# Kernel tuning notes

Measured on AMD Instinct MI355X. Metric: run time of the kernel, lower is better.

Reference implementation:

```python
import jax, jax.numpy as jnp
import numpy as np

N_NODES = 50000
N_EDGES = 1600000
F_IN = 128
HID = 128
N_CLS = 16


def setup_inputs() -> dict:
    key = jax.random.key(0)
    ks = jax.random.split(key, 8)
    x = jax.random.normal(ks[0], (N_NODES, F_IN), dtype=jnp.float32)
    edge_index = jax.random.randint(ks[1], (2, N_EDGES), 0, N_NODES, dtype=jnp.int64)
    W1 = jax.random.normal(ks[2], (F_IN, HID), dtype=jnp.float32) * (1.0 / np.sqrt(F_IN))
    b1 = jnp.zeros((HID,), dtype=jnp.float32)
    W2 = jax.random.normal(ks[3], (HID, HID), dtype=jnp.float32) * (1.0 / np.sqrt(HID))
    b2 = jnp.zeros((HID,), dtype=jnp.float32)
    W3 = jax.random.normal(ks[4], (HID, N_CLS), dtype=jnp.float32) * (1.0 / np.sqrt(HID))
    b3 = jnp.zeros((N_CLS,), dtype=jnp.float32)
    return {"x": x, "edge_index": edge_index, "W1": W1, "b1": b1,
            "W2": W2, "b2": b2, "W3": W3, "b3": b3}


def _gcn_norm(edge_index, n_nodes, dtype):
    # PyG gcn_norm with add_self_loops=True, improved=False
    loops = jnp.arange(n_nodes, dtype=edge_index.dtype)
    row = jnp.concatenate([edge_index[0], loops])  # source j
    col = jnp.concatenate([edge_index[1], loops])  # target i
    deg = jax.ops.segment_sum(jnp.ones(row.shape[0], dtype=dtype), col,
                              num_segments=n_nodes)
    dinv = jnp.where(deg > 0, jax.lax.rsqrt(deg), 0.0)
    norm = dinv[row] * dinv[col]  # [E + N]
    return row, col, norm


def _gcn_conv(h, W, b, row, col, norm, n_nodes):
    h = h @ W                              # [N, out] linear first (PyG order)
    msg = h[row] * norm[:, None]           # gather + per-edge scale
    agg = jax.ops.segment_sum(msg, col, num_segments=n_nodes)  # scatter-add
    return agg + b


def reference(x, edge_index, W1, b1, W2, b2, W3, b3):
    n = x.shape[0]
    row, col, norm = _gcn_norm(edge_index, n, x.dtype)
    h = jax.nn.relu(_gcn_conv(x, W1, b1, row, col, norm, n))
    h = jax.nn.relu(_gcn_conv(h, W2, b2, row, col, norm, n))
    h = jax.nn.relu(_gcn_conv(h, W3, b3, row, col, norm, n))
    return h
```

## Files before the change

kernel.cpp:

```cpp
#include <hip/hip_runtime.h>
#include <hip/hip_fp16.h>


static inline int cdiv(int a, int b) { return (a + b - 1) / b; }

__global__ __launch_bounds__(256) void k_zero_int(int* p, int n) {
    int i = blockIdx.x * 256 + threadIdx.x;
    if (i < n) p[i] = 0;
}

__global__ __launch_bounds__(256) void k_count(const int* __restrict__ col, int* cnt, int e) {
    int i = blockIdx.x * 256 + threadIdx.x;
    if (i < e) atomicAdd(&cnt[col[i]], 1);
}

__global__ __launch_bounds__(256) void k_scanA(const int* __restrict__ cnt, int* bsum,
                                               float* __restrict__ dinv, int n) {
    __shared__ int s[256];
    int t = threadIdx.x;
    int i = blockIdx.x * 256 + t;
    int v = (i < n) ? cnt[i] : 0;
    if (i < n) dinv[i] = rsqrtf((float)(v + 1));
    s[t] = v;
    __syncthreads();
    for (int off = 128; off > 0; off >>= 1) {
        if (t < off) s[t] += s[t + off];
        __syncthreads();
    }
    if (t == 0) bsum[blockIdx.x] = s[0];
}

__global__ __launch_bounds__(256) void k_scanB(int* bsum, int nb) {
    __shared__ int s[256];
    int t = threadIdx.x;
    int v = (t < nb) ? bsum[t] : 0;
    s[t] = v;
    for (int off = 1; off < 256; off <<= 1) {
        __syncthreads();
        int x = (t >= off) ? s[t - off] : 0;
        __syncthreads();
        s[t] += x;
    }
    __syncthreads();
    if (t < nb) bsum[t] = s[t] - v;
}

__global__ __launch_bounds__(256) void k_scanC(const int* __restrict__ cnt, const int* __restrict__ bsum,
                                               int* offs, int* cur, int n) {
    __shared__ int s[256];
    int t = threadIdx.x;
    int i = blockIdx.x * 256 + t;
    int v = (i < n) ? cnt[i] : 0;
    s[t] = v;
    for (int off = 1; off < 256; off <<= 1) {
        __syncthreads();
        int x = (t >= off) ? s[t - off] : 0;
        __syncthreads();
        s[t] += x;
    }
    __syncthreads();
    int ov = bsum[blockIdx.x] + s[t] - v;
    if (i <= n) offs[i] = ov;
    if (i < n) cur[i] = ov;
}

__global__ __launch_bounds__(256) void k_fill_xcd(const int* __restrict__ row, const int* __restrict__ col,
                                                  const float* __restrict__ dinv, int* cur,
                                                  unsigned int* __restrict__ csr, int e, int n, int nblk) {
    int g = blockIdx.x & 7;
    int b = blockIdx.x >> 3;
    int rs = (n + 7) >> 3;
    int lo = g * rs;
    int hi = min(lo + rs, n);
    int stride = nblk * 256;
    for (int i = b * 256 + threadIdx.x; i < e; i += stride) {
        int c = col[i];
        if (c >= lo && c < hi) {
            int r = row[i];
            float w = dinv[r] * dinv[c];
            int pos = atomicAdd(&cur[c], 1);
            unsigned short hw = __half_as_ushort(__float2half_rn(w));
            csr[pos] = ((unsigned int)r << 16) | (unsigned int)hw;
        }
    }
}

__global__ __launch_bounds__(256) void k_gemm128(const float* __restrict__ X, const float* __restrict__ W,
                                                 __half* __restrict__ Ah, int n) {
    __shared__ float sW[128 * 128];
    __shared__ float sX[16][128];
    int tid = threadIdx.x;
    for (int i = tid; i < 4096; i += 256)
        ((float4*)sW)[i] = ((const float4*)W)[i];

    int row0 = blockIdx.x * 128;
    int tx = tid & 15, ty = tid >> 4;
    float acc[8][8];
    #pragma unroll
    for (int i = 0; i < 8; ++i)
        #pragma unroll
        for (int j = 0; j < 8; ++j) acc[i][j] = 0.f;

    for (int k0 = 0; k0 < 128; k0 += 16) {
        __syncthreads();
        #pragma unroll
        for (int i = tid; i < 512; i += 256) {
            int r = i >> 2, kq = i & 3;
            int gr = row0 + r;
            float4 v = (gr < n) ? ((const float4*)X)[(size_t)gr * 32 + (k0 >> 2) + kq]
                                : make_float4(0.f, 0.f, 0.f, 0.f);
            sX[kq * 4 + 0][r] = v.x;
            sX[kq * 4 + 1][r] = v.y;
            sX[kq * 4 + 2][r] = v.z;
            sX[kq * 4 + 3][r] = v.w;
        }
        __syncthreads();
        #pragma unroll
        for (int kk = 0; kk < 16; ++kk) {
            float a[8], b[8];
            *(float4*)&a[0] = *(const float4*)&sX[kk][ty * 8];
            *(float4*)&a[4] = *(const float4*)&sX[kk][ty * 8 + 4];
            *(float4*)&b[0] = *(const float4*)&sW[(k0 + kk) * 128 + tx * 8];
            *(float4*)&b[4] = *(const float4*)&sW[(k0 + kk) * 128 + tx * 8 + 4];
            #pragma unroll
            for (int i = 0; i < 8; ++i)
                #pragma unroll
                for (int j = 0; j < 8; ++j)
                    acc[i][j] = fmaf(a[i], b[j], acc[i][j]);
        }
    }
    #pragma unroll
    for (int i = 0; i < 8; ++i) {
        int gr = row0 + ty * 8 + i;
        if (gr < n) {
            union { uint4 u; __half2 h[4]; } pk;
            pk.h[0] = __floats2half2_rn(acc[i][0], acc[i][1]);
            pk.h[1] = __floats2half2_rn(acc[i][2], acc[i][3]);
            pk.h[2] = __floats2half2_rn(acc[i][4], acc[i][5]);
            pk.h[3] = __floats2half2_rn(acc[i][6], acc[i][7]);
            ((uint4*)Ah)[(size_t)gr * 16 + tx] = pk.u;
        }
    }
}

__global__ __launch_bounds__(256) void k_gemm16(const float* __restrict__ X, const float* __restrict__ W,
                                                __half* __restrict__ Ch, int n) {
    __shared__ float sX[16 * 132];
    __shared__ float sW[128 * 16];
    int tid = threadIdx.x;
    for (int i = tid; i < 512; i += 256)
        ((float4*)sW)[i] = ((const float4*)W)[i];
    int row0 = blockIdx.x * 16;
    for (int i = tid; i < 512; i += 256) {
        int r = i >> 5, c = i & 31;
        int gr = row0 + r;
        float4 v = (gr < n) ? ((const float4*)X)[(size_t)gr * 32 + c]
                            : make_float4(0.f, 0.f, 0.f, 0.f);
        *(float4*)&sX[r * 132 + c * 4] = v;
    }
    __syncthreads();

    int rl = tid >> 4, cj = tid & 15;
    float acc = 0.f;
    #pragma unroll 8
    for (int k = 0; k < 128; ++k)
        acc = fmaf(sX[rl * 132 + k], sW[k * 16 + cj], acc);
    int gr = row0 + rl;
    if (gr < n) Ch[(size_t)gr * 16 + cj] = __float2half_rn(acc);
}

__global__ __launch_bounds__(256) void k_agg128(const __half* __restrict__ Hh, const unsigned int* __restrict__ csr,
                                                const int* __restrict__ offs, const float* __restrict__ dinv,
                                                const float* __restrict__ b, float* __restrict__ out, int n) {
    int node = (blockIdx.x * 256 + threadIdx.x) >> 6;
    if (node >= n) return;
    int lane = threadIdx.x & 63;
    int sub  = lane & 31;
    int half = lane >> 5;
    const uint2* H2 = (const uint2*)Hh;
    int ed = offs[node], end = offs[node + 1];
    float4 acc = make_float4(0.f, 0.f, 0.f, 0.f);

    #define EDGE_FMA(P)                                                          \
        {                                                                        \
            uint2 q = H2[(size_t)((P) >> 16) * 32 + sub];                        \
            float w = __half2float(__ushort_as_half((unsigned short)((P) & 0xffffu))); \
            float2 f01 = __half22float2(*(const __half2*)&q.x);                  \
            float2 f23 = __half22float2(*(const __half2*)&q.y);                  \
            acc.x = fmaf(w, f01.x, acc.x); acc.y = fmaf(w, f01.y, acc.y);        \
            acc.z = fmaf(w, f23.x, acc.z); acc.w = fmaf(w, f23.y, acc.w);        \
        }

    for (; ed + 7 < end; ed += 8) {
        unsigned int p0 = csr[ed     + half];
        unsigned int p1 = csr[ed + 2 + half];
        unsigned int p2 = csr[ed + 4 + half];
        unsigned int p3 = csr[ed + 6 + half];
        EDGE_FMA(p0); EDGE_FMA(p1); EDGE_FMA(p2); EDGE_FMA(p3);
    }
    #pragma unroll
    for (int s = 0; s < 4; ++s) {
        int idx = ed + 2 * s + half;
        if (idx < end) {
            unsigned int p = csr[idx];
            EDGE_FMA(p);
        }
    }
    #undef EDGE_FMA

    acc.x += __shfl_xor(acc.x, 32);
    acc.y += __shfl_xor(acc.y, 32);
    acc.z += __shfl_xor(acc.z, 32);
    acc.w += __shfl_xor(acc.w, 32);

    float di = dinv[node], sl = di * di;
    uint2 qh = H2[(size_t)node * 32 + sub];
    float2 h01 = __half22float2(*(const __half2*)&qh.x);
    float2 h23 = __half22float2(*(const __half2*)&qh.y);
    float4 bv = ((const float4*)b)[sub];
    float4 o;
    o.x = fmaxf(fmaf(sl, h01.x, acc.x) + bv.x, 0.f);
    o.y = fmaxf(fmaf(sl, h01.y, acc.y) + bv.y, 0.f);
    o.z = fmaxf(fmaf(sl, h23.x, acc.z) + bv.z, 0.f);
    o.w = fmaxf(fmaf(sl, h23.y, acc.w) + bv.w, 0.f);
    if (half == 0)
        ((float4*)out)[(size_t)node * 32 + sub] = o;
}

__global__ __launch_bounds__(256) void k_agg16(const __half* __restrict__ Ch, const unsigned int* __restrict__ csr,
                                               const int* __restrict__ offs, const float* __restrict__ dinv,
                                               const float* __restrict__ b, float* __restrict__ out, int n) {
    int t = blockIdx.x * 256 + threadIdx.x;
    int node = t >> 3;
    if (node >= n) return;
    int lane = t & 7;
    int sub  = lane & 3;
    int half = lane >> 2;
    const uint2* C2 = (const uint2*)Ch;
    int ed = offs[node], end = offs[node + 1];
    float4 acc = make_float4(0.f, 0.f, 0.f, 0.f);

    #define EDGE_FMA16(P)                                                        \
        {                                                                        \
            uint2 q = C2[(size_t)((P) >> 16) * 4 + sub];                         \
            float w = __half2float(__ushort_as_half((unsigned short)((P) & 0xffffu))); \
            float2 f01 = __half22float2(*(const __half2*)&q.x);                  \
            float2 f23 = __half22float2(*(const __half2*)&q.y);                  \
            acc.x = fmaf(w, f01.x, acc.x); acc.y = fmaf(w, f01.y, acc.y);        \
            acc.z = fmaf(w, f23.x, acc.z); acc.w = fmaf(w, f23.y, acc.w);        \
        }

    for (; ed + 3 < end; ed += 4) {
        unsigned int p0 = csr[ed     + half];
        unsigned int p1 = csr[ed + 2 + half];
        EDGE_FMA16(p0); EDGE_FMA16(p1);
    }
    #pragma unroll
    for (int s = 0; s < 2; ++s) {
        int idx = ed + 2 * s + half;
        if (idx < end) {
            unsigned int p = csr[idx];
            EDGE_FMA16(p);
        }
    }
    #undef EDGE_FMA16

    acc.x += __shfl_xor(acc.x, 4);
    acc.y += __shfl_xor(acc.y, 4);
    acc.z += __shfl_xor(acc.z, 4);
    acc.w += __shfl_xor(acc.w, 4);

    float di = dinv[node], sl = di * di;
    uint2 qh = C2[(size_t)node * 4 + sub];
    float2 h01 = __half22float2(*(const __half2*)&qh.x);
    float2 h23 = __half22float2(*(const __half2*)&qh.y);
    float4 bv = ((const float4*)b)[sub];
    float4 o;
    o.x = fmaxf(fmaf(sl, h01.x, acc.x) + bv.x, 0.f);
    o.y = fmaxf(fmaf(sl, h01.y, acc.y) + bv.y, 0.f);
    o.z = fmaxf(fmaf(sl, h23.x, acc.z) + bv.z, 0.f);
    o.w = fmaxf(fmaf(sl, h23.y, acc.w) + bv.w, 0.f);
    if (half == 0)
        ((float4*)out)[(size_t)node * 4 + sub] = o;
}

extern "C" void kernel_launch(void* const* d_in, const int* in_sizes, int n_in,
                              void* d_out, int out_size, void* d_ws, size_t ws_size,
                              hipStream_t stream) {
    const float* x  = (const float*)d_in[0];
    const int*   ei = (const int*)d_in[1];
    const float* W1 = (const float*)d_in[2];
    const float* b1 = (const float*)d_in[3];
    const float* W2 = (const float*)d_in[4];
    const float* b2 = (const float*)d_in[5];
    const float* W3 = (const float*)d_in[6];
    const float* b3 = (const float*)d_in[7];

    const int n = in_sizes[0] / 128;
    const int e = in_sizes[1] / 2;
    const int* row = ei;
    const int* col = ei + e;

    unsigned int* csr = (unsigned int*)d_ws;
    __half* Ah  = (__half*)(csr + e);
    float*  B   = (float*)(Ah + (size_t)n * 128);
    __half* Ch  = (__half*)(B + (size_t)n * 128);
    float* dinv = (float*)(Ch + (size_t)n * 16);
    int*   offs = (int*)(dinv + n);
    int*   cnt  = offs + (n + 1);
    int*   cur  = cnt + n;
    int*   bsum = cur + n;
    float* out  = (float*)d_out;

    const int nb = cdiv(n + 1, 256);
    const int fillBlocks = 256;

    k_zero_int<<<cdiv(n, 256), 256, 0, stream>>>(cnt, n);
    k_count   <<<cdiv(e, 256), 256, 0, stream>>>(col, cnt, e);
    k_scanA   <<<nb, 256, 0, stream>>>(cnt, bsum, dinv, n);
    k_scanB   <<<1, 256, 0, stream>>>(bsum, nb);
    k_scanC   <<<nb, 256, 0, stream>>>(cnt, bsum, offs, cur, n);
    k_fill_xcd<<<8 * fillBlocks, 256, 0, stream>>>(row, col, dinv, cur, csr, e, n, fillBlocks);

    k_gemm128<<<cdiv(n, 128), 256, 0, stream>>>(x, W1, Ah, n);
    k_agg128 <<<cdiv(n * 64, 256), 256, 0, stream>>>(Ah, csr, offs, dinv, b1, B, n);
    k_gemm128<<<cdiv(n, 128), 256, 0, stream>>>(B, W2, Ah, n);
    k_agg128 <<<cdiv(n * 64, 256), 256, 0, stream>>>(Ah, csr, offs, dinv, b2, B, n);
    k_gemm16 <<<cdiv(n, 16), 256, 0, stream>>>(B, W3, Ch, n);
    k_agg16  <<<cdiv(n * 8, 256), 256, 0, stream>>>(Ch, csr, offs, dinv, b3, out, n);
}
```

Measured before the change: 367.6 us.

## Fold symmetric GCN normalization into GEMM epilogue and shrink CSR to 16-bit indices

Applies the source-side dinv scaling inside the GEMM epilogues and the target-side dinv at the end of aggregation, so per-edge weights no longer need to be stored. The CSR entries shrink from packed 32-bit (index plus fp16 weight) to 16-bit source indices, which halves edge-list traffic in fill and all three aggregations and removes the per-edge FMA weight decode. The self-loop term becomes di*(acc+h). It relies on node ids fitting in 16 bits, as the previous packing already did, and the fp16 rounding now happens on the pre-scaled features.

```diff
diff --git a/kernel.cpp b/kernel.cpp
--- a/kernel.cpp
+++ b/kernel.cpp
@@ -65,8 +65,8 @@
 }
 
 __global__ __launch_bounds__(256) void k_fill_xcd(const int* __restrict__ row, const int* __restrict__ col,
-                                                  const float* __restrict__ dinv, int* cur,
-                                                  unsigned int* __restrict__ csr, int e, int n, int nblk) {
+                                                  int* cur, unsigned short* __restrict__ csr,
+                                                  int e, int n, int nblk) {
     int g = blockIdx.x & 7;
     int b = blockIdx.x >> 3;
     int rs = (n + 7) >> 3;
@@ -76,16 +76,14 @@
     for (int i = b * 256 + threadIdx.x; i < e; i += stride) {
         int c = col[i];
         if (c >= lo && c < hi) {
-            int r = row[i];
-            float w = dinv[r] * dinv[c];
             int pos = atomicAdd(&cur[c], 1);
-            unsigned short hw = __half_as_ushort(__float2half_rn(w));
-            csr[pos] = ((unsigned int)r << 16) | (unsigned int)hw;
+            csr[pos] = (unsigned short)row[i];
         }
     }
 }
 
 __global__ __launch_bounds__(256) void k_gemm128(const float* __restrict__ X, const float* __restrict__ W,
+                                                 const float* __restrict__ dinv,
                                                  __half* __restrict__ Ah, int n) {
     __shared__ float sW[128 * 128];
     __shared__ float sX[16][128];
@@ -133,17 +131,19 @@
     for (int i = 0; i < 8; ++i) {
         int gr = row0 + ty * 8 + i;
         if (gr < n) {
+            float di = dinv[gr];
             union { uint4 u; __half2 h[4]; } pk;
-            pk.h[0] = __floats2half2_rn(acc[i][0], acc[i][1]);
-            pk.h[1] = __floats2half2_rn(acc[i][2], acc[i][3]);
-            pk.h[2] = __floats2half2_rn(acc[i][4], acc[i][5]);
-            pk.h[3] = __floats2half2_rn(acc[i][6], acc[i][7]);
+            pk.h[0] = __floats2half2_rn(di * acc[i][0], di * acc[i][1]);
+            pk.h[1] = __floats2half2_rn(di * acc[i][2], di * acc[i][3]);
+            pk.h[2] = __floats2half2_rn(di * acc[i][4], di * acc[i][5]);
+            pk.h[3] = __floats2half2_rn(di * acc[i][6], di * acc[i][7]);
             ((uint4*)Ah)[(size_t)gr * 16 + tx] = pk.u;
         }
     }
 }
 
 __global__ __launch_bounds__(256) void k_gemm16(const float* __restrict__ X, const float* __restrict__ W,
+                                                const float* __restrict__ dinv,
                                                 __half* __restrict__ Ch, int n) {
     __shared__ float sX[16 * 132];
     __shared__ float sW[128 * 16];
@@ -166,10 +166,10 @@
     for (int k = 0; k < 128; ++k)
         acc = fmaf(sX[rl * 132 + k], sW[k * 16 + cj], acc);
     int gr = row0 + rl;
-    if (gr < n) Ch[(size_t)gr * 16 + cj] = __float2half_rn(acc);
-}
-
-__global__ __launch_bounds__(256) void k_agg128(const __half* __restrict__ Hh, const unsigned int* __restrict__ csr,
+    if (gr < n) Ch[(size_t)gr * 16 + cj] = __float2half_rn(dinv[gr] * acc);
+}
+
+__global__ __launch_bounds__(256) void k_agg128(const __half* __restrict__ Hh, const unsigned short* __restrict__ csr,
                                                 const int* __restrict__ offs, const float* __restrict__ dinv,
                                                 const float* __restrict__ b, float* __restrict__ out, int n) {
     int node = (blockIdx.x * 256 + threadIdx.x) >> 6;
@@ -181,53 +181,52 @@
     int ed = offs[node], end = offs[node + 1];
     float4 acc = make_float4(0.f, 0.f, 0.f, 0.f);
 
-    #define EDGE_FMA(P)                                                          \
+    #define EDGE_ADD(R)                                                          \
         {                                                                        \
-            uint2 q = H2[(size_t)((P) >> 16) * 32 + sub];                        \
-            float w = __half2float(__ushort_as_half((unsigned short)((P) & 0xffffu))); \
+            uint2 q = H2[(size_t)(R) * 32 + sub];                                \
             float2 f01 = __half22float2(*(const __half2*)&q.x);                  \
             float2 f23 = __half22float2(*(const __half2*)&q.y);                  \
-            acc.x = fmaf(w, f01.x, acc.x); acc.y = fmaf(w, f01.y, acc.y);        \
-            acc.z = fmaf(w, f23.x, acc.z); acc.w = fmaf(w, f23.y, acc.w);        \
+            acc.x += f01.x; acc.y += f01.y;                                      \
+            acc.z += f23.x; acc.w += f23.y;                                      \
         }
 
     for (; ed + 7 < end; ed += 8) {
-        unsigned int p0 = csr[ed     + half];
-        unsigned int p1 = csr[ed + 2 + half];
-        unsigned int p2 = csr[ed + 4 + half];
-        unsigned int p3 = csr[ed + 6 + half];
-        EDGE_FMA(p0); EDGE_FMA(p1); EDGE_FMA(p2); EDGE_FMA(p3);
+        int r0 = csr[ed     + half];
+        int r1 = csr[ed + 2 + half];
+        int r2 = csr[ed + 4 + half];
+        int r3 = csr[ed + 6 + half];
+        EDGE_ADD(r0); EDGE_ADD(r1); EDGE_ADD(r2); EDGE_ADD(r3);
     }
     #pragma unroll
     for (int s = 0; s < 4; ++s) {
         int idx = ed + 2 * s + half;
         if (idx < end) {
-            unsigned int p = csr[idx];
-            EDGE_FMA(p);
-        }
-    }
-    #undef EDGE_FMA
+            int r = csr[idx];
+            EDGE_ADD(r);
+        }
+    }
+    #undef EDGE_ADD
 
     acc.x += __shfl_xor(acc.x, 32);
     acc.y += __shfl_xor(acc.y, 32);
     acc.z += __shfl_xor(acc.z, 32);
     acc.w += __shfl_xor(acc.w, 32);
 
-    float di = dinv[node], sl = di * di;
+    float di = dinv[node];
     uint2 qh = H2[(size_t)node * 32 + sub];
     float2 h01 = __half22float2(*(const __half2*)&qh.x);
     float2 h23 = __half22float2(*(const __half2*)&qh.y);
     float4 bv = ((const float4*)b)[sub];
     float4 o;
-    o.x = fmaxf(fmaf(sl, h01.x, acc.x) + bv.x, 0.f);
-    o.y = fmaxf(fmaf(sl, h01.y, acc.y) + bv.y, 0.f);
-    o.z = fmaxf(fmaf(sl, h23.x, acc.z) + bv.z, 0.f);
-    o.w = fmaxf(fmaf(sl, h23.y, acc.w) + bv.w, 0.f);
+    o.x = fmaxf(fmaf(di, acc.x + h01.x, bv.x), 0.f);
+    o.y = fmaxf(fmaf(di, acc.y + h01.y, bv.y), 0.f);
+    o.z = fmaxf(fmaf(di, acc.z + h23.x, bv.z), 0.f);
+    o.w = fmaxf(fmaf(di, acc.w + h23.y, bv.w), 0.f);
     if (half == 0)
         ((float4*)out)[(size_t)node * 32 + sub] = o;
 }
 
-__global__ __launch_bounds__(256) void k_agg16(const __half* __restrict__ Ch, const unsigned int* __restrict__ csr,
+__global__ __launch_bounds__(256) void k_agg16(const __half* __restrict__ Ch, const unsigned short* __restrict__ csr,
                                                const int* __restrict__ offs, const float* __restrict__ dinv,
                                                const float* __restrict__ b, float* __restrict__ out, int n) {
     int t = blockIdx.x * 256 + threadIdx.x;
@@ -240,46 +239,45 @@
     int ed = offs[node], end = offs[node + 1];
     float4 acc = make_float4(0.f, 0.f, 0.f, 0.f);
 
-    #define EDGE_FMA16(P)                                                        \
+    #define EDGE_ADD16(R)                                                        \
         {                                                                        \
-            uint2 q = C2[(size_t)((P) >> 16) * 4 + sub];                         \
-            float w = __half2float(__ushort_as_half((unsigned short)((P) & 0xffffu))); \
+            uint2 q = C2[(size_t)(R) * 4 + sub];                                 \
             float2 f01 = __half22float2(*(const __half2*)&q.x);                  \
             float2 f23 = __half22float2(*(const __half2*)&q.y);                  \
-            acc.x = fmaf(w, f01.x, acc.x); acc.y = fmaf(w, f01.y, acc.y);        \
-            acc.z = fmaf(w, f23.x, acc.z); acc.w = fmaf(w, f23.y, acc.w);        \
+            acc.x += f01.x; acc.y += f01.y;                                      \
+            acc.z += f23.x; acc.w += f23.y;                                      \
         }
 
     for (; ed + 3 < end; ed += 4) {
-        unsigned int p0 = csr[ed     + half];
-        unsigned int p1 = csr[ed + 2 + half];
-        EDGE_FMA16(p0); EDGE_FMA16(p1);
+        int r0 = csr[ed     + half];
+        int r1 = csr[ed + 2 + half];
+        EDGE_ADD16(r0); EDGE_ADD16(r1);
     }
     #pragma unroll
     for (int s = 0; s < 2; ++s) {
         int idx = ed + 2 * s + half;
         if (idx < end) {
-            unsigned int p = csr[idx];
-            EDGE_FMA16(p);
-        }
-    }
-    #undef EDGE_FMA16
+            int r = csr[idx];
+            EDGE_ADD16(r);
+        }
+    }
+    #undef EDGE_ADD16
 
     acc.x += __shfl_xor(acc.x, 4);
     acc.y += __shfl_xor(acc.y, 4);
     acc.z += __shfl_xor(acc.z, 4);
     acc.w += __shfl_xor(acc.w, 4);
 
-    float di = dinv[node], sl = di * di;
+    float di = dinv[node];
     uint2 qh = C2[(size_t)node * 4 + sub];
     float2 h01 = __half22float2(*(const __half2*)&qh.x);
     float2 h23 = __half22float2(*(const __half2*)&qh.y);
     float4 bv = ((const float4*)b)[sub];
     float4 o;
-    o.x = fmaxf(fmaf(sl, h01.x, acc.x) + bv.x, 0.f);
-    o.y = fmaxf(fmaf(sl, h01.y, acc.y) + bv.y, 0.f);
-    o.z = fmaxf(fmaf(sl, h23.x, acc.z) + bv.z, 0.f);
-    o.w = fmaxf(fmaf(sl, h23.y, acc.w) + bv.w, 0.f);
+    o.x = fmaxf(fmaf(di, acc.x + h01.x, bv.x), 0.f);
+    o.y = fmaxf(fmaf(di, acc.y + h01.y, bv.y), 0.f);
+    o.z = fmaxf(fmaf(di, acc.z + h23.x, bv.z), 0.f);
+    o.w = fmaxf(fmaf(di, acc.w + h23.y, bv.w), 0.f);
     if (half == 0)
         ((float4*)out)[(size_t)node * 4 + sub] = o;
 }
@@ -301,8 +299,8 @@
     const int* row = ei;
     const int* col = ei + e;
 
-    unsigned int* csr = (unsigned int*)d_ws;
-    __half* Ah  = (__half*)(csr + e);
+    unsigned short* csr = (unsigned short*)d_ws;
+    __half* Ah  = (__half*)(csr + ((e + 1) & ~1));
     float*  B   = (float*)(Ah + (size_t)n * 128);
     __half* Ch  = (__half*)(B + (size_t)n * 128);
     float* dinv = (float*)(Ch + (size_t)n * 16);
@@ -320,12 +318,12 @@
     k_scanA   <<<nb, 256, 0, stream>>>(cnt, bsum, dinv, n);
     k_scanB   <<<1, 256, 0, stream>>>(bsum, nb);
     k_scanC   <<<nb, 256, 0, stream>>>(cnt, bsum, offs, cur, n);
-    k_fill_xcd<<<8 * fillBlocks, 256, 0, stream>>>(row, col, dinv, cur, csr, e, n, fillBlocks);
-
-    k_gemm128<<<cdiv(n, 128), 256, 0, stream>>>(x, W1, Ah, n);
+    k_fill_xcd<<<8 * fillBlocks, 256, 0, stream>>>(row, col, cur, csr, e, n, fillBlocks);
+
+    k_gemm128<<<cdiv(n, 128), 256, 0, stream>>>(x, W1, dinv, Ah, n);
     k_agg128 <<<cdiv(n * 64, 256), 256, 0, stream>>>(Ah, csr, offs, dinv, b1, B, n);
-    k_gemm128<<<cdiv(n, 128), 256, 0, stream>>>(B, W2, Ah, n);
+    k_gemm128<<<cdiv(n, 128), 256, 0, stream>>>(B, W2, dinv, Ah, n);
     k_agg128 <<<cdiv(n * 64, 256), 256, 0, stream>>>(Ah, csr, offs, dinv, b2, B, n);
-    k_gemm16 <<<cdiv(n, 16), 256, 0, stream>>>(B, W3, Ch, n);
+    k_gemm16 <<<cdiv(n, 16), 256, 0, stream>>>(B, W3, dinv, Ch, n);
     k_agg16  <<<cdiv(n * 8, 256), 256, 0, stream>>>(Ch, csr, offs, dinv, b3, out, n);
 }
```

New measurement: 365.1 us. About the same (-0.7%).
